# Kernel tuning notes

Hardware: AMD Instinct MI355X
Metric: run time of the kernel (lower is better)

Reference implementation:

```python
import jax, jax.numpy as jnp
import numpy as np

N, E, IN, H, OUT = 100000, 1200000, 128, 64, 2
L = 3          # num GCN layers
EPS = 1e-5     # BatchNorm eps


def setup_inputs() -> dict:
    key = jax.random.key(0)
    ks = jax.random.split(key, 14)
    x = jax.random.normal(ks[0], (N, IN), dtype=jnp.float32)
    edge_index = jax.random.randint(ks[1], (2, E), 0, N, dtype=jnp.int64)
    # GCNConv weights (glorot-ish scale) and biases
    w0 = jax.random.normal(ks[2], (IN, H), dtype=jnp.float32) / np.float32(np.sqrt(IN))
    w1 = jax.random.normal(ks[3], (H, H), dtype=jnp.float32) / np.float32(np.sqrt(H))
    w2 = jax.random.normal(ks[4], (H, H), dtype=jnp.float32) / np.float32(np.sqrt(H))
    biases = jax.random.normal(ks[5], (L, H), dtype=jnp.float32) * 0.01
    # BatchNorm (eval mode): gamma, beta, running mean/var per layer
    gamma = jnp.ones((L, H), jnp.float32) + 0.1 * jax.random.normal(ks[6], (L, H), dtype=jnp.float32)
    beta = 0.1 * jax.random.normal(ks[7], (L, H), dtype=jnp.float32)
    run_mean = 0.1 * jax.random.normal(ks[8], (L, H), dtype=jnp.float32)
    run_var = 0.5 + jax.random.uniform(ks[9], (L, H), dtype=jnp.float32)  # strictly positive
    # classifier
    cls_w = jax.random.normal(ks[10], (H, OUT), dtype=jnp.float32) / np.float32(np.sqrt(H))
    cls_b = jnp.zeros((OUT,), jnp.float32)
    return {"x": x, "edge_index": edge_index, "w0": w0, "w1": w1, "w2": w2,
            "biases": biases, "gamma": gamma, "beta": beta,
            "run_mean": run_mean, "run_var": run_var,
            "cls_w": cls_w, "cls_b": cls_b}


def reference(x, edge_index, w0, w1, w2, biases, gamma, beta, run_mean, run_var, cls_w, cls_b):
    n = x.shape[0]
    loop = jnp.arange(n, dtype=edge_index.dtype)
    row = jnp.concatenate([edge_index[0], loop])  # source (with self-loops)
    col = jnp.concatenate([edge_index[1], loop])  # target (with self-loops)
    # symmetric normalization: D^{-1/2} (A+I) D^{-1/2}, degree on target index
    deg = jax.ops.segment_sum(jnp.ones(row.shape, x.dtype), col, num_segments=n)
    dinv = jnp.where(deg > 0, jax.lax.rsqrt(deg), 0.0)
    norm = dinv[row] * dinv[col]  # [E+N]

    h = x
    for l, w in enumerate((w0, w1, w2)):
        h = h @ w                                                   # [N,H]
        msg = norm[:, None] * h[row]                                # gather + scale [E+N,H]
        h = jax.ops.segment_sum(msg, col, num_segments=n) + biases[l]
        # BatchNorm1d (eval) + ReLU
        scale = gamma[l] * jax.lax.rsqrt(run_var[l] + EPS)
        h = jax.nn.relu((h - run_mean[l]) * scale + beta[l])
        # dropout is identity in eval mode
    return h @ cls_w + cls_b  # [N, OUT]
```

## Files before the change

kernel.cpp:

```cpp
#include <hip/hip_runtime.h>
#include <hip/hip_fp16.h>

#define EPS 1e-5f
#define ABITS 9
#define ACHUNK 4096

typedef _Float16 half8 __attribute__((ext_vector_type(8)));
typedef float floatx4 __attribute__((ext_vector_type(4)));


__global__ __launch_bounds__(256) void bucketA1_kernel(const int* __restrict__ ei, int E,
                                                       int* __restrict__ bucket_count) {
    __shared__ int hist[256];
    int t = threadIdx.x;
    hist[t] = 0;
    __syncthreads();
    int e0 = blockIdx.x * ACHUNK;
    int e1 = e0 + ACHUNK; if (e1 > E) e1 = E;
    for (int e = e0 + t; e < e1; e += 256)
        atomicAdd(&hist[ei[E + e] >> ABITS], 1);
    __syncthreads();
    int h = hist[t];
    if (h) atomicAdd(&bucket_count[t], h);
}

__global__ __launch_bounds__(256) void bscan_kernel(const int* __restrict__ bucket_count,
                                                    int* __restrict__ bucket_off, int* __restrict__ bucket_cursor,
                                                    int* __restrict__ rowptr, int nbuckets, int n) {
    __shared__ int s[256];
    int t = threadIdx.x;
    int v = bucket_count[t];
    s[t] = v;
    __syncthreads();
    for (int off = 1; off < 256; off <<= 1) {
        int u = (t >= off) ? s[t - off] : 0;
        __syncthreads();
        s[t] += u;
        __syncthreads();
    }
    int excl = s[t] - v;
    if (t < nbuckets) { bucket_off[t] = excl; bucket_cursor[t] = excl; }
    if (t == 255) { bucket_off[nbuckets] = s[255]; rowptr[n] = s[255]; }
}

__global__ __launch_bounds__(256) void bucketA2_kernel(const int* __restrict__ ei, int E,
                                                       int* __restrict__ bucket_cursor, int2* __restrict__ tmp) {
    __shared__ int hist[256], lbase[256], lcur[256];
    int t = threadIdx.x;
    hist[t] = 0; lcur[t] = 0;
    __syncthreads();
    int e0 = blockIdx.x * ACHUNK;
    int e1 = e0 + ACHUNK; if (e1 > E) e1 = E;
    for (int e = e0 + t; e < e1; e += 256)
        atomicAdd(&hist[ei[E + e] >> ABITS], 1);
    __syncthreads();
    int h = hist[t];
    if (h) lbase[t] = atomicAdd(&bucket_cursor[t], h);
    __syncthreads();
    for (int e = e0 + t; e < e1; e += 256) {
        int r = ei[e], c = ei[E + e];
        int b = c >> ABITS;
        int l = atomicAdd(&lcur[b], 1);
        tmp[lbase[b] + l] = make_int2(r, c);
    }
}

__global__ __launch_bounds__(256) void bucketB1_kernel(const int2* __restrict__ tmp,
                                                       const int* __restrict__ bucket_off,
                                                       int* __restrict__ rowptr, float* __restrict__ dinv,
                                                       int n) {
    __shared__ int cnt[512];
    __shared__ int ps[256];
    int b = blockIdx.x, t = threadIdx.x;
    int n0 = b << ABITS;
    int cntN = n - n0; if (cntN > 512) cntN = 512;
    cnt[t] = 0; cnt[t + 256] = 0;
    __syncthreads();
    int start = bucket_off[b], end = bucket_off[b + 1];
    for (int idx = start + t; idx < end; idx += 256)
        atomicAdd(&cnt[tmp[idx].y - n0], 1);
    __syncthreads();
    int c0 = cnt[2 * t], c1 = cnt[2 * t + 1];
    int s = c0 + c1;
    ps[t] = s;
    __syncthreads();
    for (int off = 1; off < 256; off <<= 1) {
        int u = (t >= off) ? ps[t - off] : 0;
        __syncthreads();
        ps[t] += u;
        __syncthreads();
    }
    int excl = ps[t] - s;
    int i0 = 2 * t, i1 = 2 * t + 1;
    if (i0 < cntN) {
        rowptr[n0 + i0] = start + excl;
        dinv[n0 + i0] = rsqrtf((float)(c0 + 1));
    }
    if (i1 < cntN) {
        rowptr[n0 + i1] = start + excl + c0;
        dinv[n0 + i1] = rsqrtf((float)(c1 + 1));
    }
}

__global__ __launch_bounds__(256) void bucketB2_kernel(const int2* __restrict__ tmp,
                                                       const int* __restrict__ bucket_off,
                                                       const int* __restrict__ rowptr,
                                                       const float* __restrict__ dinv, int2* __restrict__ csrw,
                                                       int n) {
    __shared__ int lrp[512];
    __shared__ float ldv[512];
    __shared__ int lcur[512];
    int b = blockIdx.x, t = threadIdx.x;
    int n0 = b << ABITS;
    int cntN = n - n0; if (cntN > 512) cntN = 512;
    for (int i = t; i < cntN; i += 256) {
        lrp[i] = rowptr[n0 + i];
        ldv[i] = dinv[n0 + i];
        lcur[i] = 0;
    }
    __syncthreads();
    int start = bucket_off[b], end = bucket_off[b + 1];
    for (int idx = start + t; idx < end; idx += 256) {
        int2 st = tmp[idx];
        int lt = st.y - n0;
        int l = atomicAdd(&lcur[lt], 1);
        float w = dinv[st.x] * ldv[lt];
        csrw[lrp[lt] + l] = make_int2(st.x, __float_as_int(w));
    }
}


template <int K>
__global__ __launch_bounds__(256) void gemm_kernel(const float* __restrict__ A, const float* __restrict__ W,
                                                   __half* __restrict__ out, int n) {
    const int KP = K + 8;
    __shared__ _Float16 Ah[64 * (K + 8)];
    __shared__ _Float16 Wt[64 * (K + 8)];
    int tid = threadIdx.x;

    for (int idx = tid; idx < K * 64; idx += 256) {
        int k = idx >> 6, c = idx & 63;
        Wt[c * KP + k] = (_Float16)W[idx];
    }
    int row0 = blockIdx.x * 64;
    const float* Ab = A + (size_t)row0 * K;
    int limit = (n - row0) * K; if (limit > 64 * K) limit = 64 * K;
    for (int f = tid * 4; f < 64 * K; f += 1024) {
        float4 v = make_float4(0.f, 0.f, 0.f, 0.f);
        if (f + 3 < limit) {
            v = *(const float4*)(Ab + f);
        } else {
            if (f + 0 < limit) v.x = Ab[f + 0];
            if (f + 1 < limit) v.y = Ab[f + 1];
            if (f + 2 < limit) v.z = Ab[f + 2];
        }
        int row = f / K, k = f % K;
        _Float16* dst = Ah + row * KP + k;
        dst[0] = (_Float16)v.x; dst[1] = (_Float16)v.y;
        dst[2] = (_Float16)v.z; dst[3] = (_Float16)v.w;
    }
    __syncthreads();

    int w = tid >> 6, lane = tid & 63;
    int m = lane & 15, quad = lane >> 4;
    const _Float16* Aw = Ah + (size_t)(w * 16 + m) * KP + quad * 8;
    const _Float16* Bw = Wt + (size_t)m * KP + quad * 8;

    floatx4 acc0 = {0.f, 0.f, 0.f, 0.f}, acc1 = acc0, acc2 = acc0, acc3 = acc0;
    for (int k0 = 0; k0 < K; k0 += 32) {
        half8 a  = *(const half8*)(Aw + k0);
        half8 b0 = *(const half8*)(Bw + 0 * 16 * KP + k0);
        half8 b1 = *(const half8*)(Bw + 1 * 16 * KP + k0);
        half8 b2 = *(const half8*)(Bw + 2 * 16 * KP + k0);
        half8 b3 = *(const half8*)(Bw + 3 * 16 * KP + k0);
        acc0 = __builtin_amdgcn_mfma_f32_16x16x32_f16(a, b0, acc0, 0, 0, 0);
        acc1 = __builtin_amdgcn_mfma_f32_16x16x32_f16(a, b1, acc1, 0, 0, 0);
        acc2 = __builtin_amdgcn_mfma_f32_16x16x32_f16(a, b2, acc2, 0, 0, 0);
        acc3 = __builtin_amdgcn_mfma_f32_16x16x32_f16(a, b3, acc3, 0, 0, 0);
    }

    int rbase = row0 + w * 16 + quad * 4;
#pragma unroll
    for (int r = 0; r < 4; ++r) {
        int row = rbase + r;
        if (row < n) {
            __half* o = out + (size_t)row * 64 + m;
            o[0]  = __float2half(acc0[r]);
            o[16] = __float2half(acc1[r]);
            o[32] = __float2half(acc2[r]);
            o[48] = __float2half(acc3[r]);
        }
    }
}


__device__ __forceinline__ void agg_acc8(float4& lo, float4& hi, float wgt, uint4 raw) {
    float2 p0 = __half22float2(*(const __half2*)&raw.x);
    float2 p1 = __half22float2(*(const __half2*)&raw.y);
    float2 p2 = __half22float2(*(const __half2*)&raw.z);
    float2 p3 = __half22float2(*(const __half2*)&raw.w);
    lo.x += wgt * p0.x; lo.y += wgt * p0.y; lo.z += wgt * p1.x; lo.w += wgt * p1.y;
    hi.x += wgt * p2.x; hi.y += wgt * p2.y; hi.z += wgt * p3.x; hi.w += wgt * p3.y;
}

template <bool FUSE_CLS>
__global__ __launch_bounds__(256) void agg_kernel(const __half* __restrict__ t, const float* __restrict__ dinv,
                                                  const int* __restrict__ rowptr, const int2* __restrict__ csrw,
                                                  const float* __restrict__ bias, const float* __restrict__ gamma,
                                                  const float* __restrict__ beta, const float* __restrict__ mean,
                                                  const float* __restrict__ var, float* __restrict__ out,
                                                  const float* __restrict__ cls_w, const float* __restrict__ cls_b,
                                                  int n) {
    int wave = threadIdx.x >> 6;
    int lane = threadIdx.x & 63;
    int g = lane >> 3;
    int fl = lane & 7;
    int i = (blockIdx.x * (blockDim.x >> 6) + wave) * 8 + g;
    if (i >= n) return;

    float4 lo = make_float4(0.f, 0.f, 0.f, 0.f);
    float4 hi = make_float4(0.f, 0.f, 0.f, 0.f);

    float di = dinv[i];
    uint4 self = *(const uint4*)(t + (size_t)i * 64 + fl * 8);
    agg_acc8(lo, hi, di * di, self);

    int e0 = rowptr[i], e1 = rowptr[i + 1];
    int e = e0;
    for (; e + 4 <= e1; e += 4) {
        int2 a0 = csrw[e + 0], a1 = csrw[e + 1], a2 = csrw[e + 2], a3 = csrw[e + 3];
        uint4 r0 = *(const uint4*)(t + (size_t)a0.x * 64 + fl * 8);
        uint4 r1 = *(const uint4*)(t + (size_t)a1.x * 64 + fl * 8);
        uint4 r2 = *(const uint4*)(t + (size_t)a2.x * 64 + fl * 8);
        uint4 r3 = *(const uint4*)(t + (size_t)a3.x * 64 + fl * 8);
        agg_acc8(lo, hi, __int_as_float(a0.y), r0);
        agg_acc8(lo, hi, __int_as_float(a1.y), r1);
        agg_acc8(lo, hi, __int_as_float(a2.y), r2);
        agg_acc8(lo, hi, __int_as_float(a3.y), r3);
    }
    if (e + 2 <= e1) {
        int2 a0 = csrw[e + 0], a1 = csrw[e + 1];
        uint4 r0 = *(const uint4*)(t + (size_t)a0.x * 64 + fl * 8);
        uint4 r1 = *(const uint4*)(t + (size_t)a1.x * 64 + fl * 8);
        agg_acc8(lo, hi, __int_as_float(a0.y), r0);
        agg_acc8(lo, hi, __int_as_float(a1.y), r1);
        e += 2;
    }
    if (e < e1) {
        int2 a = csrw[e];
        uint4 r = *(const uint4*)(t + (size_t)a.x * 64 + fl * 8);
        agg_acc8(lo, hi, __int_as_float(a.y), r);
    }

    float4 bbL = ((const float4*)bias)[2 * fl],  bbH = ((const float4*)bias)[2 * fl + 1];
    float4 ggL = ((const float4*)gamma)[2 * fl], ggH = ((const float4*)gamma)[2 * fl + 1];
    float4 beL = ((const float4*)beta)[2 * fl],  beH = ((const float4*)beta)[2 * fl + 1];
    float4 mmL = ((const float4*)mean)[2 * fl],  mmH = ((const float4*)mean)[2 * fl + 1];
    float4 vvL = ((const float4*)var)[2 * fl],   vvH = ((const float4*)var)[2 * fl + 1];
    float4 resL, resH;
    resL.x = fmaxf((lo.x + bbL.x - mmL.x) * (ggL.x * rsqrtf(vvL.x + EPS)) + beL.x, 0.f);
    resL.y = fmaxf((lo.y + bbL.y - mmL.y) * (ggL.y * rsqrtf(vvL.y + EPS)) + beL.y, 0.f);
    resL.z = fmaxf((lo.z + bbL.z - mmL.z) * (ggL.z * rsqrtf(vvL.z + EPS)) + beL.z, 0.f);
    resL.w = fmaxf((lo.w + bbL.w - mmL.w) * (ggL.w * rsqrtf(vvL.w + EPS)) + beL.w, 0.f);
    resH.x = fmaxf((hi.x + bbH.x - mmH.x) * (ggH.x * rsqrtf(vvH.x + EPS)) + beH.x, 0.f);
    resH.y = fmaxf((hi.y + bbH.y - mmH.y) * (ggH.y * rsqrtf(vvH.y + EPS)) + beH.y, 0.f);
    resH.z = fmaxf((hi.z + bbH.z - mmH.z) * (ggH.z * rsqrtf(vvH.z + EPS)) + beH.z, 0.f);
    resH.w = fmaxf((hi.w + bbH.w - mmH.w) * (ggH.w * rsqrtf(vvH.w + EPS)) + beH.w, 0.f);

    if (!FUSE_CLS) {
        ((float4*)out)[(size_t)i * 16 + 2 * fl + 0] = resL;
        ((float4*)out)[(size_t)i * 16 + 2 * fl + 1] = resH;
    } else {
        const float4* cw = (const float4*)cls_w;
        float4 cwA = cw[4 * fl + 0], cwB = cw[4 * fl + 1], cwC = cw[4 * fl + 2], cwD = cw[4 * fl + 3];
        float c0 = resL.x * cwA.x + resL.y * cwA.z + resL.z * cwB.x + resL.w * cwB.z
                 + resH.x * cwC.x + resH.y * cwC.z + resH.z * cwD.x + resH.w * cwD.z;
        float c1 = resL.x * cwA.y + resL.y * cwA.w + resL.z * cwB.y + resL.w * cwB.w
                 + resH.x * cwC.y + resH.y * cwC.w + resH.z * cwD.y + resH.w * cwD.w;
        for (int off = 4; off > 0; off >>= 1) {
            c0 += __shfl_xor(c0, off);
            c1 += __shfl_xor(c1, off);
        }
        if (fl == 0) {
            out[(size_t)i * 2 + 0] = c0 + cls_b[0];
            out[(size_t)i * 2 + 1] = c1 + cls_b[1];
        }
    }
}


extern "C" void kernel_launch(void* const* d_in, const int* in_sizes, int n_in,
                              void* d_out, int out_size, void* d_ws, size_t ws_size,
                              hipStream_t stream) {
    const float* x      = (const float*)d_in[0];
    const int*   ei     = (const int*)d_in[1];
    const float* w0     = (const float*)d_in[2];
    const float* w1     = (const float*)d_in[3];
    const float* w2     = (const float*)d_in[4];
    const float* biases = (const float*)d_in[5];
    const float* gamma  = (const float*)d_in[6];
    const float* beta   = (const float*)d_in[7];
    const float* rmean  = (const float*)d_in[8];
    const float* rvar   = (const float*)d_in[9];
    const float* cls_w  = (const float*)d_in[10];
    const float* cls_b  = (const float*)d_in[11];
    float* out = (float*)d_out;

    const int IN = 128, H = 64;
    const int N = in_sizes[0] / IN;
    const int E = in_sizes[1] / 2;

    char* p = (char*)d_ws;
    auto carve = [&](size_t bytes) { void* q = (void*)p; p += (bytes + 255) & ~(size_t)255; return q; };
    float* dinv    = (float*)carve((size_t)N * 4);
    int*   rowptr  = (int*)carve((size_t)(N + 1) * 4);
    int2*  tmp     = (int2*)carve((size_t)E * 8);
    int2*  csrw    = (int2*)carve((size_t)E * 8);
    int*   bucket_count  = (int*)carve((size_t)256 * 4);
    int*   bucket_off    = (int*)carve((size_t)257 * 4);
    int*   bucket_cursor = (int*)carve((size_t)256 * 4);
    __half* tbuf   = (__half*)carve((size_t)N * H * 2);
    float* hbuf    = (float*)carve((size_t)N * H * 4);

    int nbuckets = (N + (1 << ABITS) - 1) >> ABITS;
    int na = (E + ACHUNK - 1) / ACHUNK;

    hipMemsetAsync(bucket_count, 0, (size_t)256 * 4, stream);
    bucketA1_kernel<<<na, 256, 0, stream>>>(ei, E, bucket_count);
    bscan_kernel<<<1, 256, 0, stream>>>(bucket_count, bucket_off, bucket_cursor, rowptr, nbuckets, N);
    bucketA2_kernel<<<na, 256, 0, stream>>>(ei, E, bucket_cursor, tmp);
    bucketB1_kernel<<<nbuckets, 256, 0, stream>>>(tmp, bucket_off, rowptr, dinv, N);
    bucketB2_kernel<<<nbuckets, 256, 0, stream>>>(tmp, bucket_off, rowptr, dinv, csrw, N);

    int gemm_grid = (N + 63) / 64;
    int agg_grid  = (N + 31) / 32;

    gemm_kernel<128><<<gemm_grid, 256, 0, stream>>>(x, w0, tbuf, N);
    agg_kernel<false><<<agg_grid, 256, 0, stream>>>(tbuf, dinv, rowptr, csrw,
        biases + 0, gamma + 0, beta + 0, rmean + 0, rvar + 0, hbuf, nullptr, nullptr, N);
    gemm_kernel<64><<<gemm_grid, 256, 0, stream>>>(hbuf, w1, tbuf, N);
    agg_kernel<false><<<agg_grid, 256, 0, stream>>>(tbuf, dinv, rowptr, csrw,
        biases + H, gamma + H, beta + H, rmean + H, rvar + H, hbuf, nullptr, nullptr, N);
    gemm_kernel<64><<<gemm_grid, 256, 0, stream>>>(hbuf, w2, tbuf, N);
    agg_kernel<true><<<agg_grid, 256, 0, stream>>>(tbuf, dinv, rowptr, csrw,
        biases + 2 * H, gamma + 2 * H, beta + 2 * H, rmean + 2 * H, rvar + 2 * H, out, cls_w, cls_b, N);
}
```

Before: 283.6 us.

## Factor normalization into GEMM epilogue, drop edge weights, store hidden in fp16

Source-side dinv scaling moves into the GEMM epilogue and target-side dinv into the aggregation epilogue, so the CSR stores only int source indices. The two bucket passes merge into one kernel that caches each bucket's edges in LDS. Hidden activations between layers are stored as fp16 instead of fp32, and the gather loop is unrolled to 8. Together these cut edge-list and activation traffic and one launch, but add fp16 rounding of intermediates and large LDS use in the bucket kernel.

Result: faster. 273.9 us (-3.4%).

```diff
diff --git a/kernel.cpp b/kernel.cpp
--- a/kernel.cpp
+++ b/kernel.cpp
@@ -4,6 +4,7 @@
 #define EPS 1e-5f
 #define ABITS 9
 #define ACHUNK 4096
+#define BMAX 8192
 
 typedef _Float16 half8 __attribute__((ext_vector_type(8)));
 typedef float floatx4 __attribute__((ext_vector_type(4)));
@@ -65,20 +66,28 @@
     }
 }
 
-__global__ __launch_bounds__(256) void bucketB1_kernel(const int2* __restrict__ tmp,
-                                                       const int* __restrict__ bucket_off,
-                                                       int* __restrict__ rowptr, float* __restrict__ dinv,
-                                                       int n) {
+__global__ __launch_bounds__(256) void bucketB_kernel(const int2* __restrict__ tmp,
+                                                      const int* __restrict__ bucket_off,
+                                                      int* __restrict__ rowptr, float* __restrict__ dinv,
+                                                      int* __restrict__ csr, int n) {
+    __shared__ int2 edg[BMAX];
     __shared__ int cnt[512];
     __shared__ int ps[256];
+    __shared__ int lrp[512];
     int b = blockIdx.x, t = threadIdx.x;
     int n0 = b << ABITS;
     int cntN = n - n0; if (cntN > 512) cntN = 512;
+    int start = bucket_off[b], end = bucket_off[b + 1];
+    int ne = end - start;
+    bool inlds = ne <= BMAX;
     cnt[t] = 0; cnt[t + 256] = 0;
-    __syncthreads();
-    int start = bucket_off[b], end = bucket_off[b + 1];
-    for (int idx = start + t; idx < end; idx += 256)
-        atomicAdd(&cnt[tmp[idx].y - n0], 1);
+    if (inlds)
+        for (int idx = t; idx < ne; idx += 256) edg[idx] = tmp[start + idx];
+    __syncthreads();
+    for (int idx = t; idx < ne; idx += 256) {
+        int dst = inlds ? edg[idx].y : tmp[start + idx].y;
+        atomicAdd(&cnt[dst - n0], 1);
+    }
     __syncthreads();
     int c0 = cnt[2 * t], c1 = cnt[2 * t + 1];
     int s = c0 + c1;
@@ -91,48 +100,30 @@
         __syncthreads();
     }
     int excl = ps[t] - s;
-    int i0 = 2 * t, i1 = 2 * t + 1;
-    if (i0 < cntN) {
-        rowptr[n0 + i0] = start + excl;
-        dinv[n0 + i0] = rsqrtf((float)(c0 + 1));
-    }
-    if (i1 < cntN) {
-        rowptr[n0 + i1] = start + excl + c0;
-        dinv[n0 + i1] = rsqrtf((float)(c1 + 1));
-    }
-}
-
-__global__ __launch_bounds__(256) void bucketB2_kernel(const int2* __restrict__ tmp,
-                                                       const int* __restrict__ bucket_off,
-                                                       const int* __restrict__ rowptr,
-                                                       const float* __restrict__ dinv, int2* __restrict__ csrw,
-                                                       int n) {
-    __shared__ int lrp[512];
-    __shared__ float ldv[512];
-    __shared__ int lcur[512];
-    int b = blockIdx.x, t = threadIdx.x;
-    int n0 = b << ABITS;
-    int cntN = n - n0; if (cntN > 512) cntN = 512;
-    for (int i = t; i < cntN; i += 256) {
-        lrp[i] = rowptr[n0 + i];
-        ldv[i] = dinv[n0 + i];
-        lcur[i] = 0;
-    }
-    __syncthreads();
-    int start = bucket_off[b], end = bucket_off[b + 1];
-    for (int idx = start + t; idx < end; idx += 256) {
-        int2 st = tmp[idx];
+    if (2 * t < cntN) {
+        lrp[2 * t] = start + excl;
+        rowptr[n0 + 2 * t] = start + excl;
+        dinv[n0 + 2 * t] = rsqrtf((float)(c0 + 1));
+    }
+    if (2 * t + 1 < cntN) {
+        lrp[2 * t + 1] = start + excl + c0;
+        rowptr[n0 + 2 * t + 1] = start + excl + c0;
+        dinv[n0 + 2 * t + 1] = rsqrtf((float)(c1 + 1));
+    }
+    cnt[2 * t] = 0; cnt[2 * t + 1] = 0;
+    __syncthreads();
+    for (int idx = t; idx < ne; idx += 256) {
+        int2 st = inlds ? edg[idx] : tmp[start + idx];
         int lt = st.y - n0;
-        int l = atomicAdd(&lcur[lt], 1);
-        float w = dinv[st.x] * ldv[lt];
-        csrw[lrp[lt] + l] = make_int2(st.x, __float_as_int(w));
-    }
-}
-
-
-template <int K>
-__global__ __launch_bounds__(256) void gemm_kernel(const float* __restrict__ A, const float* __restrict__ W,
-                                                   __half* __restrict__ out, int n) {
+        int l = atomicAdd(&cnt[lt], 1);
+        csr[lrp[lt] + l] = st.x;
+    }
+}
+
+
+template <int K, typename TIN>
+__global__ __launch_bounds__(256) void gemm_kernel(const TIN* __restrict__ A, const float* __restrict__ W,
+                                                   const float* __restrict__ dinv, __half* __restrict__ out, int n) {
     const int KP = K + 8;
     __shared__ _Float16 Ah[64 * (K + 8)];
     __shared__ _Float16 Wt[64 * (K + 8)];
@@ -143,21 +134,38 @@
         Wt[c * KP + k] = (_Float16)W[idx];
     }
     int row0 = blockIdx.x * 64;
-    const float* Ab = A + (size_t)row0 * K;
+    const TIN* Ab = A + (size_t)row0 * K;
     int limit = (n - row0) * K; if (limit > 64 * K) limit = 64 * K;
-    for (int f = tid * 4; f < 64 * K; f += 1024) {
-        float4 v = make_float4(0.f, 0.f, 0.f, 0.f);
-        if (f + 3 < limit) {
-            v = *(const float4*)(Ab + f);
-        } else {
-            if (f + 0 < limit) v.x = Ab[f + 0];
-            if (f + 1 < limit) v.y = Ab[f + 1];
-            if (f + 2 < limit) v.z = Ab[f + 2];
-        }
-        int row = f / K, k = f % K;
-        _Float16* dst = Ah + row * KP + k;
-        dst[0] = (_Float16)v.x; dst[1] = (_Float16)v.y;
-        dst[2] = (_Float16)v.z; dst[3] = (_Float16)v.w;
+
+    if constexpr (sizeof(TIN) == 4) {
+        for (int f = tid * 4; f < 64 * K; f += 1024) {
+            float4 v = make_float4(0.f, 0.f, 0.f, 0.f);
+            if (f + 3 < limit) {
+                v = *(const float4*)((const float*)Ab + f);
+            } else {
+                if (f + 0 < limit) v.x = ((const float*)Ab)[f + 0];
+                if (f + 1 < limit) v.y = ((const float*)Ab)[f + 1];
+                if (f + 2 < limit) v.z = ((const float*)Ab)[f + 2];
+            }
+            int row = f / K, k = f % K;
+            _Float16* dst = Ah + row * KP + k;
+            dst[0] = (_Float16)v.x; dst[1] = (_Float16)v.y;
+            dst[2] = (_Float16)v.z; dst[3] = (_Float16)v.w;
+        }
+    } else {
+        for (int f = tid * 8; f < 64 * K; f += 2048) {
+            uint4 v = make_uint4(0, 0, 0, 0);
+            if (f + 7 < limit) {
+                v = *(const uint4*)((const __half*)Ab + f);
+            } else {
+                const __half* hp = (const __half*)Ab;
+                __half tmp8[8];
+                for (int j = 0; j < 8; ++j) tmp8[j] = (f + j < limit) ? hp[f + j] : __half(0);
+                v = *(const uint4*)tmp8;
+            }
+            int row = f / K, k = f % K;
+            *(uint4*)(Ah + row * KP + k) = v;
+        }
     }
     __syncthreads();
 
@@ -184,31 +192,33 @@
     for (int r = 0; r < 4; ++r) {
         int row = rbase + r;
         if (row < n) {
+            float dv = dinv[row];
             __half* o = out + (size_t)row * 64 + m;
-            o[0]  = __float2half(acc0[r]);
-            o[16] = __float2half(acc1[r]);
-            o[32] = __float2half(acc2[r]);
-            o[48] = __float2half(acc3[r]);
-        }
-    }
-}
-
-
-__device__ __forceinline__ void agg_acc8(float4& lo, float4& hi, float wgt, uint4 raw) {
+            o[0]  = __float2half(acc0[r] * dv);
+            o[16] = __float2half(acc1[r] * dv);
+            o[32] = __float2half(acc2[r] * dv);
+            o[48] = __float2half(acc3[r] * dv);
+        }
+    }
+}
+
+
+__device__ __forceinline__ void agg_add8(float4& lo, float4& hi, uint4 raw) {
     float2 p0 = __half22float2(*(const __half2*)&raw.x);
     float2 p1 = __half22float2(*(const __half2*)&raw.y);
     float2 p2 = __half22float2(*(const __half2*)&raw.z);
     float2 p3 = __half22float2(*(const __half2*)&raw.w);
-    lo.x += wgt * p0.x; lo.y += wgt * p0.y; lo.z += wgt * p1.x; lo.w += wgt * p1.y;
-    hi.x += wgt * p2.x; hi.y += wgt * p2.y; hi.z += wgt * p3.x; hi.w += wgt * p3.y;
+    lo.x += p0.x; lo.y += p0.y; lo.z += p1.x; lo.w += p1.y;
+    hi.x += p2.x; hi.y += p2.y; hi.z += p3.x; hi.w += p3.y;
 }
 
 template <bool FUSE_CLS>
 __global__ __launch_bounds__(256) void agg_kernel(const __half* __restrict__ t, const float* __restrict__ dinv,
-                                                  const int* __restrict__ rowptr, const int2* __restrict__ csrw,
+                                                  const int* __restrict__ rowptr, const int* __restrict__ csr,
                                                   const float* __restrict__ bias, const float* __restrict__ gamma,
                                                   const float* __restrict__ beta, const float* __restrict__ mean,
-                                                  const float* __restrict__ var, float* __restrict__ out,
+                                                  const float* __restrict__ var, __half* __restrict__ hout,
+                                                  float* __restrict__ fout,
                                                   const float* __restrict__ cls_w, const float* __restrict__ cls_b,
                                                   int n) {
     int wave = threadIdx.x >> 6;
@@ -221,36 +231,50 @@
     float4 lo = make_float4(0.f, 0.f, 0.f, 0.f);
     float4 hi = make_float4(0.f, 0.f, 0.f, 0.f);
 
-    float di = dinv[i];
     uint4 self = *(const uint4*)(t + (size_t)i * 64 + fl * 8);
-    agg_acc8(lo, hi, di * di, self);
+    agg_add8(lo, hi, self);
 
     int e0 = rowptr[i], e1 = rowptr[i + 1];
     int e = e0;
-    for (; e + 4 <= e1; e += 4) {
-        int2 a0 = csrw[e + 0], a1 = csrw[e + 1], a2 = csrw[e + 2], a3 = csrw[e + 3];
-        uint4 r0 = *(const uint4*)(t + (size_t)a0.x * 64 + fl * 8);
-        uint4 r1 = *(const uint4*)(t + (size_t)a1.x * 64 + fl * 8);
-        uint4 r2 = *(const uint4*)(t + (size_t)a2.x * 64 + fl * 8);
-        uint4 r3 = *(const uint4*)(t + (size_t)a3.x * 64 + fl * 8);
-        agg_acc8(lo, hi, __int_as_float(a0.y), r0);
-        agg_acc8(lo, hi, __int_as_float(a1.y), r1);
-        agg_acc8(lo, hi, __int_as_float(a2.y), r2);
-        agg_acc8(lo, hi, __int_as_float(a3.y), r3);
+    for (; e + 8 <= e1; e += 8) {
+        int s0 = csr[e + 0], s1 = csr[e + 1], s2 = csr[e + 2], s3 = csr[e + 3];
+        int s4 = csr[e + 4], s5 = csr[e + 5], s6 = csr[e + 6], s7 = csr[e + 7];
+        uint4 r0 = *(const uint4*)(t + (size_t)s0 * 64 + fl * 8);
+        uint4 r1 = *(const uint4*)(t + (size_t)s1 * 64 + fl * 8);
+        uint4 r2 = *(const uint4*)(t + (size_t)s2 * 64 + fl * 8);
+        uint4 r3 = *(const uint4*)(t + (size_t)s3 * 64 + fl * 8);
+        uint4 r4 = *(const uint4*)(t + (size_t)s4 * 64 + fl * 8);
+        uint4 r5 = *(const uint4*)(t + (size_t)s5 * 64 + fl * 8);
+        uint4 r6 = *(const uint4*)(t + (size_t)s6 * 64 + fl * 8);
+        uint4 r7 = *(const uint4*)(t + (size_t)s7 * 64 + fl * 8);
+        agg_add8(lo, hi, r0); agg_add8(lo, hi, r1); agg_add8(lo, hi, r2); agg_add8(lo, hi, r3);
+        agg_add8(lo, hi, r4); agg_add8(lo, hi, r5); agg_add8(lo, hi, r6); agg_add8(lo, hi, r7);
+    }
+    if (e + 4 <= e1) {
+        int s0 = csr[e + 0], s1 = csr[e + 1], s2 = csr[e + 2], s3 = csr[e + 3];
+        uint4 r0 = *(const uint4*)(t + (size_t)s0 * 64 + fl * 8);
+        uint4 r1 = *(const uint4*)(t + (size_t)s1 * 64 + fl * 8);
+        uint4 r2 = *(const uint4*)(t + (size_t)s2 * 64 + fl * 8);
+        uint4 r3 = *(const uint4*)(t + (size_t)s3 * 64 + fl * 8);
+        agg_add8(lo, hi, r0); agg_add8(lo, hi, r1); agg_add8(lo, hi, r2); agg_add8(lo, hi, r3);
+        e += 4;
     }
     if (e + 2 <= e1) {
-        int2 a0 = csrw[e + 0], a1 = csrw[e + 1];
-        uint4 r0 = *(const uint4*)(t + (size_t)a0.x * 64 + fl * 8);
-        uint4 r1 = *(const uint4*)(t + (size_t)a1.x * 64 + fl * 8);
-        agg_acc8(lo, hi, __int_as_float(a0.y), r0);
-        agg_acc8(lo, hi, __int_as_float(a1.y), r1);
+        int s0 = csr[e + 0], s1 = csr[e + 1];
+        uint4 r0 = *(const uint4*)(t + (size_t)s0 * 64 + fl * 8);
+        uint4 r1 = *(const uint4*)(t + (size_t)s1 * 64 + fl * 8);
+        agg_add8(lo, hi, r0); agg_add8(lo, hi, r1);
         e += 2;
     }
     if (e < e1) {
-        int2 a = csrw[e];
-        uint4 r = *(const uint4*)(t + (size_t)a.x * 64 + fl * 8);
-        agg_acc8(lo, hi, __int_as_float(a.y), r);
-    }
+        int s0 = csr[e];
+        uint4 r0 = *(const uint4*)(t + (size_t)s0 * 64 + fl * 8);
+        agg_add8(lo, hi, r0);
+    }
+
+    float di = dinv[i];
+    lo.x *= di; lo.y *= di; lo.z *= di; lo.w *= di;
+    hi.x *= di; hi.y *= di; hi.z *= di; hi.w *= di;
 
     float4 bbL = ((const float4*)bias)[2 * fl],  bbH = ((const float4*)bias)[2 * fl + 1];
     float4 ggL = ((const float4*)gamma)[2 * fl], ggH = ((const float4*)gamma)[2 * fl + 1];
@@ -268,8 +292,14 @@
     resH.w = fmaxf((hi.w + bbH.w - mmH.w) * (ggH.w * rsqrtf(vvH.w + EPS)) + beH.w, 0.f);
 
     if (!FUSE_CLS) {
-        ((float4*)out)[(size_t)i * 16 + 2 * fl + 0] = resL;
-        ((float4*)out)[(size_t)i * 16 + 2 * fl + 1] = resH;
+        __half2 h0 = __floats2half2_rn(resL.x, resL.y);
+        __half2 h1 = __floats2half2_rn(resL.z, resL.w);
+        __half2 h2 = __floats2half2_rn(resH.x, resH.y);
+        __half2 h3 = __floats2half2_rn(resH.z, resH.w);
+        uint4 pk;
+        pk.x = *(unsigned*)&h0; pk.y = *(unsigned*)&h1;
+        pk.z = *(unsigned*)&h2; pk.w = *(unsigned*)&h3;
+        ((uint4*)hout)[(size_t)i * 8 + fl] = pk;
     } else {
         const float4* cw = (const float4*)cls_w;
         float4 cwA = cw[4 * fl + 0], cwB = cw[4 * fl + 1], cwC = cw[4 * fl + 2], cwD = cw[4 * fl + 3];
@@ -282,8 +312,8 @@
             c1 += __shfl_xor(c1, off);
         }
         if (fl == 0) {
-            out[(size_t)i * 2 + 0] = c0 + cls_b[0];
-            out[(size_t)i * 2 + 1] = c1 + cls_b[1];
+            fout[(size_t)i * 2 + 0] = c0 + cls_b[0];
+            fout[(size_t)i * 2 + 1] = c1 + cls_b[1];
         }
     }
 }
@@ -315,12 +345,12 @@
     float* dinv    = (float*)carve((size_t)N * 4);
     int*   rowptr  = (int*)carve((size_t)(N + 1) * 4);
     int2*  tmp     = (int2*)carve((size_t)E * 8);
-    int2*  csrw    = (int2*)carve((size_t)E * 8);
+    int*   csr     = (int*)carve((size_t)E * 4);
     int*   bucket_count  = (int*)carve((size_t)256 * 4);
     int*   bucket_off    = (int*)carve((size_t)257 * 4);
     int*   bucket_cursor = (int*)carve((size_t)256 * 4);
     __half* tbuf   = (__half*)carve((size_t)N * H * 2);
-    float* hbuf    = (float*)carve((size_t)N * H * 4);
+    __half* hbuf   = (__half*)carve((size_t)N * H * 2);
 
     int nbuckets = (N + (1 << ABITS) - 1) >> ABITS;
     int na = (E + ACHUNK - 1) / ACHUNK;
@@ -329,19 +359,18 @@
     bucketA1_kernel<<<na, 256, 0, stream>>>(ei, E, bucket_count);
     bscan_kernel<<<1, 256, 0, stream>>>(bucket_count, bucket_off, bucket_cursor, rowptr, nbuckets, N);
     bucketA2_kernel<<<na, 256, 0, stream>>>(ei, E, bucket_cursor, tmp);
-    bucketB1_kernel<<<nbuckets, 256, 0, stream>>>(tmp, bucket_off, rowptr, dinv, N);
-    bucketB2_kernel<<<nbuckets, 256, 0, stream>>>(tmp, bucket_off, rowptr, dinv, csrw, N);
+    bucketB_kernel<<<nbuckets, 256, 0, stream>>>(tmp, bucket_off, rowptr, dinv, csr, N);
 
     int gemm_grid = (N + 63) / 64;
     int agg_grid  = (N + 31) / 32;
 
-    gemm_kernel<128><<<gemm_grid, 256, 0, stream>>>(x, w0, tbuf, N);
-    agg_kernel<false><<<agg_grid, 256, 0, stream>>>(tbuf, dinv, rowptr, csrw,
-        biases + 0, gamma + 0, beta + 0, rmean + 0, rvar + 0, hbuf, nullptr, nullptr, N);
-    gemm_kernel<64><<<gemm_grid, 256, 0, stream>>>(hbuf, w1, tbuf, N);
-    agg_kernel<false><<<agg_grid, 256, 0, stream>>>(tbuf, dinv, rowptr, csrw,
-        biases + H, gamma + H, beta + H, rmean + H, rvar + H, hbuf, nullptr, nullptr, N);
-    gemm_kernel<64><<<gemm_grid, 256, 0, stream>>>(hbuf, w2, tbuf, N);
-    agg_kernel<true><<<agg_grid, 256, 0, stream>>>(tbuf, dinv, rowptr, csrw,
-        biases + 2 * H, gamma + 2 * H, beta + 2 * H, rmean + 2 * H, rvar + 2 * H, out, cls_w, cls_b, N);
-}
+    gemm_kernel<128, float><<<gemm_grid, 256, 0, stream>>>(x, w0, dinv, tbuf, N);
+    agg_kernel<false><<<agg_grid, 256, 0, stream>>>(tbuf, dinv, rowptr, csr,
+        biases + 0, gamma + 0, beta + 0, rmean + 0, rvar + 0, hbuf, nullptr, nullptr, nullptr, N);
+    gemm_kernel<64, __half><<<gemm_grid, 256, 0, stream>>>(hbuf, w1, dinv, tbuf, N);
+    agg_kernel<false><<<agg_grid, 256, 0, stream>>>(tbuf, dinv, rowptr, csr,
+        biases + H, gamma + H, beta + H, rmean + H, rvar + H, hbuf, nullptr, nullptr, nullptr, N);
+    gemm_kernel<64, __half><<<gemm_grid, 256, 0, stream>>>(hbuf, w2, dinv, tbuf, N);
+    agg_kernel<true><<<agg_grid, 256, 0, stream>>>(tbuf, dinv, rowptr, csr,
+        biases + 2 * H, gamma + 2 * H, beta + 2 * H, rmean + 2 * H, rvar + 2 * H, nullptr, out, cls_w, cls_b, N);
+}
```
